# Kernel tuning notes

Measured on AMD Instinct MI355X. Metric: run time of the kernel, lower is better.

## Reference

```python
import jax, jax.numpy as jnp
import numpy as np

MIN_PS = 4
MAX_PS = 16


def _enforce(mb):
    # mb: (L,) bool candidate boundaries (merge_signal < 0.7-quantile)
    # Faithful re-implementation of _enforce_patch_size_constraints:
    # walk boundaries left->right, skip segments < MIN_PS (start not advanced),
    # accept otherwise, and insert ceil(ps/MAX_PS)-1 evenly spaced splits for
    # oversized segments. seq_len-1 is always appended as a candidate.
    L = mb.shape[0]
    pos = jnp.arange(L, dtype=jnp.int32)
    cand = mb | (pos == L - 1)

    def fwd_step(start, inp):
        p, is_c = inp
        ps = p - start
        acc = is_c & (ps >= MIN_PS)
        k = jnp.where(acc, (ps + MAX_PS - 1) // MAX_PS, jnp.int32(1))
        sz = jnp.maximum(jnp.where(acc, ps // k, jnp.int32(1)), 1)
        new_start = jnp.where(acc, p, start)
        return new_start, (acc, start, sz, k)

    _, (acc, seg_start, sz, k) = jax.lax.scan(fwd_step, jnp.int32(0), (pos, cand))

    # Reverse scan: propagate each accepted boundary's (start, split_size, num_splits)
    # back to the interior positions of its segment so splits can be placed in parallel.
    def rev_step(carry, inp):
        a, s, z, kk = inp
        cs, cz, ck, cv = carry
        out = (cs, cz, ck, cv)
        ncarry = (jnp.where(a, s, cs), jnp.where(a, z, cz), jnp.where(a, kk, ck), cv | a)
        return ncarry, out

    init = (jnp.int32(0), jnp.int32(1), jnp.int32(1), jnp.bool_(False))
    _, (fs, fz, fk, fv) = jax.lax.scan(rev_step, init, (acc, seg_start, sz, k), reverse=True)
    r = pos - fs
    j = r // fz
    split = fv & (r > 0) & (r % fz == 0) & (j >= 1) & (j <= fk - 1)
    return acc | split


def reference(x, attention_mask, W1, b1, W2, b2, Wc, bc, Wb1, bb1, Wb2, bb2):
    B, L, D = x.shape
    # content scorer: Linear -> ReLU -> Linear -> Sigmoid
    content = jax.nn.sigmoid(jax.nn.relu(x @ W1 + b1) @ W2 + b2)[..., 0]  # (B, L)
    # grouped Conv1d(d, d//2, k=3, pad=1, groups=d//4)
    xc = jnp.transpose(x, (0, 2, 1))  # (B, D, L)
    pf = jax.lax.conv_general_dilated(xc, Wc, (1,), ((1, 1),),
                                      feature_group_count=D // 4,
                                      dimension_numbers=('NCH', 'OIH', 'NCH'))
    pf = jnp.transpose(pf + bc[None, :, None], (0, 2, 1))  # (B, L, D//2)
    comb = jnp.concatenate([x, pf], axis=-1)
    bscore = jax.nn.sigmoid(jax.nn.relu(comb @ Wb1 + bb1) @ Wb2 + bb2)[..., 0]  # (B, L)
    signal = content * (1.0 - bscore) * attention_mask
    thr = jnp.quantile(signal, 0.7, axis=1, keepdims=True)
    mb = signal < thr
    new_b = jax.vmap(_enforce)(mb)  # (B, L) bool, new_b[:,0] is always False

    # segment id per token = inclusive cumsum of boundaries
    seg = jnp.cumsum(new_b.astype(jnp.int32), axis=1)
    seg_flat = (seg + jnp.arange(B, dtype=jnp.int32)[:, None] * L).reshape(-1)
    NS = B * L
    xm = x * attention_mask[..., None]
    e = jnp.sum(xm * xm, axis=-1).reshape(-1)  # softmax logits = ||token||^2
    m = jax.ops.segment_max(e, seg_flat, num_segments=NS)
    w = jnp.exp(e - m[seg_flat])
    denom = jax.ops.segment_sum(w, seg_flat, num_segments=NS)
    wn = w / denom[seg_flat]
    merged = jax.ops.segment_sum(xm.reshape(-1, D) * wn[:, None], seg_flat,
                                 num_segments=NS).reshape(B, L, D)
    # segment_boundaries: 1 for every segment except the first, zero padding
    n_last = seg[:, -1]
    p = jnp.arange(L)
    seg_bounds = ((p[None, :] >= 1) & (p[None, :] <= n_last[:, None])).astype(jnp.float32)
    return merged, seg_bounds


def setup_inputs() -> dict:
    key = jax.random.key(0)
    B, L, D = 4, 8192, 512
    ks = jax.random.split(key, 8)
    s = 0.02
    return {
        'x': jax.random.normal(ks[0], (B, L, D), jnp.float32),
        'attention_mask': jnp.ones((B, L), jnp.float32),
        'W1': jax.random.normal(ks[1], (D, D // 4), jnp.float32) * s,
        'b1': jnp.zeros((D // 4,), jnp.float32),
        'W2': jax.random.normal(ks[2], (D // 4, 1), jnp.float32) * s,
        'b2': jnp.zeros((1,), jnp.float32),
        'Wc': jax.random.normal(ks[3], (D // 2, 4, 3), jnp.float32) * s,
        'bc': jnp.zeros((D // 2,), jnp.float32),
        'Wb1': jax.random.normal(ks[4], (D + D // 2, D // 4), jnp.float32) * s,
        'bb1': jnp.zeros((D // 4,), jnp.float32),
        'Wb2': jax.random.normal(ks[5], (D // 4, 1), jnp.float32) * s,
        'bb2': jnp.zeros((1,), jnp.float32),
    }
```

## Files before the change

### kernel.cpp

```cpp
#include <hip/hip_runtime.h>
#include <math.h>

#define B_  4
#define L_  8192
#define D_  512
#define BL_ (B_*L_)
#define TOK 32
#define XS  36
#define KC  16
#define NCH (D_/KC)

__global__ __launch_bounds__(256, 4) void k_signal(
    const float* __restrict__ x, const float* __restrict__ mask,
    const float* __restrict__ W1, const float* __restrict__ b1,
    const float* __restrict__ W2, const float* __restrict__ b2,
    const float* __restrict__ Wc, const float* __restrict__ bc,
    const float* __restrict__ Wb1, const float* __restrict__ bb1,
    const float* __restrict__ Wb2, const float* __restrict__ bb2,
    float* __restrict__ signal, float* __restrict__ e)
{
  __shared__ float ws1[KC][128];
  __shared__ float wsb[KC][128];
  __shared__ float wsp[8][128];
  __shared__ float xt[KC][XS];
  __shared__ float pf[8][XS];

  const int t   = threadIdx.x;
  const int blk = blockIdx.x;
  const int b   = blk >> 8;
  const int l0  = (blk & 255) * TOK;
  const float* xb = x + (size_t)b * L_ * D_;

  const int jq = t & 31, tw = t >> 5;
  const int j0 = jq << 2, tok0 = tw << 2;

  const int stok = t >> 2, skk = t & 3;
  const int oo_c  = t >> 5;
  const int tokc  = t & 31;
  const int cb_c  = (oo_c >> 1) << 2;

  const int row = t >> 5, c4 = (t & 31) << 2;

  float a1[4][4], a2[4][4];
#pragma unroll
  for (int i = 0; i < 4; ++i)
#pragma unroll
    for (int j = 0; j < 4; ++j) { a1[i][j] = 0.f; a2[i][j] = 0.f; }
  float esacc = 0.f;

  float4 r_w1a, r_w1b, r_wba, r_wbb, r_wp, r_x;
  float4 r_wc0, r_wc1, r_wc2;
  float  r_bc;

#define ISSUE_LOADS(cc) do {                                                    \
    const int kc_ = (cc) << 4;                                                  \
    r_w1a = *reinterpret_cast<const float4*>(W1 + (size_t)(kc_ + row) * 128 + c4);       \
    r_w1b = *reinterpret_cast<const float4*>(W1 + (size_t)(kc_ + 8 + row) * 128 + c4);   \
    r_wba = *reinterpret_cast<const float4*>(Wb1 + (size_t)(kc_ + row) * 128 + c4);      \
    r_wbb = *reinterpret_cast<const float4*>(Wb1 + (size_t)(kc_ + 8 + row) * 128 + c4);  \
    r_wp  = *reinterpret_cast<const float4*>(Wb1 + (size_t)(512 + ((cc) << 3) + row) * 128 + c4); \
    {                                                                           \
      const int o_ = ((cc) << 3) + oo_c;                                        \
      const float* wcp_ = Wc + o_ * 12;                                         \
      r_wc0 = *reinterpret_cast<const float4*>(wcp_);                           \
      r_wc1 = *reinterpret_cast<const float4*>(wcp_ + 4);                       \
      r_wc2 = *reinterpret_cast<const float4*>(wcp_ + 8);                       \
      r_bc  = bc[o_];                                                           \
    }                                                                           \
    if (t < 128) {                                                              \
      r_x = *reinterpret_cast<const float4*>(xb + (size_t)(l0 + stok) * D_ + kc_ + (skk << 2)); \
    } else if (t < 136) {                                                       \
      const int q_ = t - 128;                                                   \
      const int l_ = (q_ >> 2) ? (l0 + TOK) : (l0 - 1);                         \
      r_x = make_float4(0.f, 0.f, 0.f, 0.f);                                    \
      if (l_ >= 0 && l_ < L_)                                                   \
        r_x = *reinterpret_cast<const float4*>(xb + (size_t)l_ * D_ + kc_ + ((q_ & 3) << 2)); \
    }                                                                           \
  } while (0)

#define WRITE_LDS() do {                                                        \
    *reinterpret_cast<float4*>(&ws1[row][c4]) = r_w1a;                          \
    *reinterpret_cast<float4*>(&ws1[8 + row][c4]) = r_w1b;                      \
    *reinterpret_cast<float4*>(&wsb[row][c4]) = r_wba;                          \
    *reinterpret_cast<float4*>(&wsb[8 + row][c4]) = r_wbb;                      \
    *reinterpret_cast<float4*>(&wsp[row][c4]) = r_wp;                           \
    if (t < 128) {                                                              \
      esacc = fmaf(r_x.x, r_x.x, esacc); esacc = fmaf(r_x.y, r_x.y, esacc);     \
      esacc = fmaf(r_x.z, r_x.z, esacc); esacc = fmaf(r_x.w, r_x.w, esacc);     \
      const int r_ = skk << 2;                                                  \
      xt[r_ + 0][stok] = r_x.x; xt[r_ + 1][stok] = r_x.y;                       \
      xt[r_ + 2][stok] = r_x.z; xt[r_ + 3][stok] = r_x.w;                       \
    } else if (t < 136) {                                                       \
      const int q_ = t - 128; const int kk_ = q_ & 3;                           \
      const int col_ = TOK + (q_ >> 2); const int r_ = kk_ << 2;                \
      xt[r_ + 0][col_] = r_x.x; xt[r_ + 1][col_] = r_x.y;                       \
      xt[r_ + 2][col_] = r_x.z; xt[r_ + 3][col_] = r_x.w;                       \
    }                                                                           \
  } while (0)

  ISSUE_LOADS(0);
  WRITE_LDS();

  for (int c = 0; c < NCH; ++c) {
    __syncthreads();

    {
      const float wc12[12] = {r_wc0.x, r_wc0.y, r_wc0.z, r_wc0.w,
                              r_wc1.x, r_wc1.y, r_wc1.z, r_wc1.w,
                              r_wc2.x, r_wc2.y, r_wc2.z, r_wc2.w};
      float acc = r_bc;
      const int tm1 = (tokc == 0) ? TOK : tokc - 1;
      const int tp1 = (tokc == TOK - 1) ? TOK + 1 : tokc + 1;
#pragma unroll
      for (int i = 0; i < 4; ++i) {
        const float* rowp = &xt[cb_c + i][0];
        acc = fmaf(rowp[tm1],  wc12[i * 3 + 0], acc);
        acc = fmaf(rowp[tokc], wc12[i * 3 + 1], acc);
        acc = fmaf(rowp[tp1],  wc12[i * 3 + 2], acc);
      }
      pf[oo_c][tokc] = acc;
    }

    if (c + 1 < NCH) ISSUE_LOADS(c + 1);

#pragma unroll 4
    for (int k = 0; k < KC; ++k) {
      const float4 w1 = *reinterpret_cast<const float4*>(&ws1[k][j0]);
      const float4 wb = *reinterpret_cast<const float4*>(&wsb[k][j0]);
      const float4 xv = *reinterpret_cast<const float4*>(&xt[k][tok0]);
      const float xs4[4] = {xv.x, xv.y, xv.z, xv.w};
#pragma unroll
      for (int i = 0; i < 4; ++i) {
        a1[i][0] = fmaf(xs4[i], w1.x, a1[i][0]);
        a1[i][1] = fmaf(xs4[i], w1.y, a1[i][1]);
        a1[i][2] = fmaf(xs4[i], w1.z, a1[i][2]);
        a1[i][3] = fmaf(xs4[i], w1.w, a1[i][3]);
        a2[i][0] = fmaf(xs4[i], wb.x, a2[i][0]);
        a2[i][1] = fmaf(xs4[i], wb.y, a2[i][1]);
        a2[i][2] = fmaf(xs4[i], wb.z, a2[i][2]);
        a2[i][3] = fmaf(xs4[i], wb.w, a2[i][3]);
      }
    }
    __syncthreads();

#pragma unroll 4
    for (int oo = 0; oo < 8; ++oo) {
      const float4 wp = *reinterpret_cast<const float4*>(&wsp[oo][j0]);
      const float4 pv = *reinterpret_cast<const float4*>(&pf[oo][tok0]);
      const float ps4[4] = {pv.x, pv.y, pv.z, pv.w};
#pragma unroll
      for (int i = 0; i < 4; ++i) {
        a2[i][0] = fmaf(ps4[i], wp.x, a2[i][0]);
        a2[i][1] = fmaf(ps4[i], wp.y, a2[i][1]);
        a2[i][2] = fmaf(ps4[i], wp.z, a2[i][2]);
        a2[i][3] = fmaf(ps4[i], wp.w, a2[i][3]);
      }
    }

    if (c + 1 < NCH) {
      __syncthreads();
      WRITE_LDS();
    }
  }

  {
    float b1v[4], w2v[4], bbv[4], wv2[4];
#pragma unroll
    for (int jj = 0; jj < 4; ++jj) {
      b1v[jj] = b1[j0 + jj];  w2v[jj] = W2[j0 + jj];
      bbv[jj] = bb1[j0 + jj]; wv2[jj] = Wb2[j0 + jj];
    }
    const float bias2 = b2[0], biasb2 = bb2[0];
#pragma unroll
    for (int i = 0; i < 4; ++i) {
      float p1 = 0.f, p2 = 0.f;
#pragma unroll
      for (int jj = 0; jj < 4; ++jj) {
        const float h1 = a1[i][jj] + b1v[jj];
        if (h1 > 0.f) p1 = fmaf(h1, w2v[jj], p1);
        const float h2 = a2[i][jj] + bbv[jj];
        if (h2 > 0.f) p2 = fmaf(h2, wv2[jj], p2);
      }
#pragma unroll
      for (int off = 1; off < 32; off <<= 1) {
        p1 += __shfl_xor(p1, off, 64);
        p2 += __shfl_xor(p2, off, 64);
      }
      if (jq == 0) {
        const int gi = b * L_ + l0 + tok0 + i;
        const float content = 1.f / (1.f + expf(-(p1 + bias2)));
        const float bscore  = 1.f / (1.f + expf(-(p2 + biasb2)));
        signal[gi] = content * (1.f - bscore) * mask[gi];
      }
    }
  }

  if (t < 128) {
    float es = esacc;
    es += __shfl_xor(es, 1, 64);
    es += __shfl_xor(es, 2, 64);
    if (skk == 0) {
      const int gi = b * L_ + l0 + stok;
      const float m = mask[gi];
      e[gi] = m * m * es;
    }
  }
#undef ISSUE_LOADS
#undef WRITE_LDS
}

__device__ __forceinline__ int chain_sim(unsigned long long w, int from) {
  int last = -1;
  while (from < 64) {
    const unsigned long long m = w & (~0ull << from);
    if (m == 0ull) break;
    const int p = __ffsll(m) - 1;
    last = p;
    from = p + 4;
  }
  return last;
}

__global__ __launch_bounds__(1024) void k_select(
    const float* __restrict__ signal,
    int* __restrict__ starts, int* __restrict__ nlast, float* __restrict__ bounds)
{
  __shared__ unsigned int bins[4][256];
  __shared__ unsigned int sel_prefix;
  __shared__ int sel_rank;
  __shared__ float sh_thr;
  __shared__ unsigned int wmin[16];
  __shared__ int wcnt[16];
  __shared__ unsigned long long cw[128];
  __shared__ unsigned char nb[L_];
  __shared__ signed char tbl[128][4];
  __shared__ int st_in[128];
  __shared__ int tsum[256];
  __shared__ int offs[257];

  const int b = blockIdx.x, t = threadIdx.x;
  const int wv = t >> 6, lane = t & 63;
  const float* s = signal + b * L_;

  float val[8];
  unsigned int key[8];
#pragma unroll
  for (int i = 0; i < 8; ++i) {
    val[i] = s[(i << 10) + t];
    const unsigned int u = __float_as_uint(val[i]);
    key[i] = (u & 0x80000000u) ? ~u : (u | 0x80000000u);
  }

  if (t == 0) { sel_prefix = 0u; sel_rank = 5733; }
  __syncthreads();
  for (int round = 0; round < 4; ++round) {
    reinterpret_cast<unsigned int*>(bins)[t] = 0u;
    __syncthreads();
    const unsigned int pre = sel_prefix;
    const int shift = 24 - 8 * round;
    if (round < 2) {
#pragma unroll
      for (int i = 0; i < 8; ++i) {
        const bool act = (round == 0) || ((key[i] >> (shift + 8)) == pre);
        const unsigned int bin = (key[i] >> shift) & 255u;
        unsigned long long peers = __ballot(act);
#pragma unroll
        for (int bit = 0; bit < 8; ++bit) {
          const bool myb = (bin >> bit) & 1;
          const unsigned long long bb = __ballot(act && myb);
          peers &= myb ? bb : ~bb;
        }
        if (act) {
          const int leader = __ffsll(peers) - 1;
          if (lane == leader)
            atomicAdd(&bins[wv >> 2][bin], (unsigned int)__popcll(peers));
        }
      }
    } else {
#pragma unroll
      for (int i = 0; i < 8; ++i) {
        if ((key[i] >> (shift + 8)) == pre)
          atomicAdd(&bins[wv >> 2][(key[i] >> shift) & 255u], 1u);
      }
    }
    __syncthreads();
    if (t < 256)
      bins[0][t] = bins[0][t] + bins[1][t] + bins[2][t] + bins[3][t];
    __syncthreads();
    if (t < 64) {
      const unsigned int c0 = bins[0][(t << 2) + 0], c1 = bins[0][(t << 2) + 1];
      const unsigned int c2 = bins[0][(t << 2) + 2], c3 = bins[0][(t << 2) + 3];
      const unsigned int lsum = c0 + c1 + c2 + c3;
      unsigned int run = lsum;
#pragma unroll
      for (int off = 1; off < 64; off <<= 1) {
        const unsigned int v = __shfl_up(run, off, 64);
        if (t >= off) run += v;
      }
      const int r = sel_rank;
      if (r >= (int)(run - lsum) && r < (int)run) {
        int rr = r - (int)(run - lsum);
        unsigned int cbin;
        if (rr < (int)c0) { cbin = 0; }
        else if (rr < (int)(c0 + c1)) { cbin = 1; rr -= (int)c0; }
        else if (rr < (int)(c0 + c1 + c2)) { cbin = 2; rr -= (int)(c0 + c1); }
        else { cbin = 3; rr -= (int)(c0 + c1 + c2); }
        sel_rank = rr;
        sel_prefix = (pre << 8) | ((unsigned int)(t << 2) | cbin);
      }
    }
    __syncthreads();
  }
  const unsigned int k0 = sel_prefix;

  {
    int cle = 0;
    unsigned int mgt = 0xFFFFFFFFu;
#pragma unroll
    for (int i = 0; i < 8; ++i) {
      if (key[i] <= k0) ++cle;
      else mgt = min(mgt, key[i]);
    }
#pragma unroll
    for (int off = 1; off < 64; off <<= 1) {
      cle += __shfl_xor(cle, off, 64);
      mgt = min(mgt, (unsigned int)__shfl_xor((int)mgt, off, 64));
    }
    if (lane == 0) { wcnt[wv] = cle; wmin[wv] = mgt; }
    __syncthreads();
    if (t == 0) {
      int C = 0; unsigned int M = 0xFFFFFFFFu;
      for (int g = 0; g < 16; ++g) { C += wcnt[g]; M = min(M, wmin[g]); }
      const unsigned int k1 = (C >= 5735) ? k0 : M;
      const unsigned int u0 = (k0 & 0x80000000u) ? (k0 & 0x7fffffffu) : ~k0;
      const unsigned int u1 = (k1 & 0x80000000u) ? (k1 & 0x7fffffffu) : ~k1;
      const float v0 = __uint_as_float(u0);
      const float v1 = __uint_as_float(u1);
      const float g = 0.7f * 8191.0f - 5733.0f;
      sh_thr = v0 + g * (v1 - v0);
    }
    __syncthreads();
  }
  const float thr = sh_thr;

#pragma unroll
  for (int i = 0; i < 8; ++i) {
    const unsigned long long m = __ballot(val[i] < thr);
    if (lane == 0) cw[(i << 4) + wv] = m;
  }
  {
    const int base = t << 3;
#pragma unroll
    for (int i = 0; i < 8; ++i) nb[base + i] = 0;
  }
  __syncthreads();
  if (t == 0) cw[127] |= (1ull << 63);
  __syncthreads();

  if (t < 512) {
    const int blk = t >> 2, cls = t & 3;
    tbl[blk][cls] = (signed char)chain_sim(cw[blk], cls);
  }
  __syncthreads();

  if (t == 0) {
    int st = 0;
    for (int blk = 0; blk < 128; ++blk) {
      const int bs = blk << 6;
      st_in[blk] = st;
      int pl;
      if (blk == 0) {
        pl = chain_sim(cw[0], 4);
      } else {
        int off = st + 4 - bs;
        if (off < 0) off = 0;
        pl = tbl[blk][off];
      }
      if (pl >= 0) st = bs + pl;
    }
  }
  __syncthreads();

  if (t < 128) {
    const int bs = t << 6;
    const unsigned long long w = cw[t];
    int st = st_in[t];
    int from = st + 4 - bs;
    if (from < 0) from = 0;
    while (from < 64) {
      const unsigned long long m = w & (~0ull << from);
      if (m == 0ull) break;
      const int p_rel = __ffsll(m) - 1;
      const int p = bs + p_rel;
      nb[p] = 1;
      const int ps = p - st;
      const int k = (ps + 15) >> 4;
      if (k > 1) {
        int sz = ps / k; if (sz < 1) sz = 1;
        for (int j = 1; j < k; ++j) nb[st + j * sz] = 1;
      }
      st = p;
      from = p_rel + 4;
    }
  }
  __syncthreads();

  if (t < 256) {
    const int base = t << 5;
    int ls = 0;
    for (int i = 0; i < 32; ++i) ls += nb[base + i];
    tsum[t] = ls;
  }
  __syncthreads();
  if (t == 0) {
    int r = 0;
    for (int i = 0; i < 256; ++i) { offs[i] = r; r += tsum[i]; }
    offs[256] = r;
  }
  __syncthreads();
  if (t < 256) {
    const int base = t << 5;
    int run = offs[t];
    for (int i = 0; i < 32; ++i) {
      run += nb[base + i];
      if (nb[base + i]) starts[b * L_ + run] = base + i;
    }
  }
  if (t == 0) { starts[b * L_ + 0] = 0; nlast[b] = offs[256]; }
  __syncthreads();
  const int total = offs[256];
  for (int i = t; i < L_; i += 1024)
    bounds[b * L_ + i] = (i >= 1 && i <= total) ? 1.0f : 0.0f;
}

__global__ __launch_bounds__(64) void k_merge(const float* __restrict__ x,
    const float* __restrict__ mask, const float* __restrict__ e,
    const int* __restrict__ starts, const int* __restrict__ nlast,
    float* __restrict__ merged)
{
  const int idx = blockIdx.x;
  const int b   = idx >> 13;
  const int sid = idx & (L_ - 1);
  const int n = nlast[b];
  const int lane = threadIdx.x;
  const int c0 = lane << 3;
  float* o = merged + (size_t)(b * L_ + sid) * D_ + c0;
  if (sid > n) {
    const float4 z = make_float4(0.f, 0.f, 0.f, 0.f);
    reinterpret_cast<float4*>(o)[0] = z;
    reinterpret_cast<float4*>(o)[1] = z;
    return;
  }
  const int t0 = starts[b * L_ + sid];
  const int t1 = (sid < n) ? starts[b * L_ + sid + 1] : L_;
  const float* eb = e + b * L_;

  float mx = -INFINITY;
  for (int p = t0; p < t1; ++p) mx = fmaxf(mx, eb[p]);
  float den = 0.f;
  for (int p = t0; p < t1; ++p) den += expf(eb[p] - mx);

  float acc[8] = {0,0,0,0,0,0,0,0};
  for (int p = t0; p < t1; ++p) {
    const float wn = expf(eb[p] - mx) / den;
    const float sc = wn * mask[b * L_ + p];
    const float* xr = x + ((size_t)(b * L_ + p)) * D_ + c0;
    const float4 u0 = reinterpret_cast<const float4*>(xr)[0];
    const float4 u1 = reinterpret_cast<const float4*>(xr)[1];
    acc[0] = fmaf(sc, u0.x, acc[0]); acc[1] = fmaf(sc, u0.y, acc[1]);
    acc[2] = fmaf(sc, u0.z, acc[2]); acc[3] = fmaf(sc, u0.w, acc[3]);
    acc[4] = fmaf(sc, u1.x, acc[4]); acc[5] = fmaf(sc, u1.y, acc[5]);
    acc[6] = fmaf(sc, u1.z, acc[6]); acc[7] = fmaf(sc, u1.w, acc[7]);
  }
  reinterpret_cast<float4*>(o)[0] = make_float4(acc[0], acc[1], acc[2], acc[3]);
  reinterpret_cast<float4*>(o)[1] = make_float4(acc[4], acc[5], acc[6], acc[7]);
}

extern "C" void kernel_launch(void* const* d_in, const int* in_sizes, int n_in,
                              void* d_out, int out_size, void* d_ws, size_t ws_size,
                              hipStream_t stream) {
  (void)in_sizes; (void)n_in; (void)out_size; (void)ws_size;
  const float* x    = (const float*)d_in[0];
  const float* mask = (const float*)d_in[1];
  const float* W1   = (const float*)d_in[2];
  const float* b1   = (const float*)d_in[3];
  const float* W2   = (const float*)d_in[4];
  const float* b2   = (const float*)d_in[5];
  const float* Wc   = (const float*)d_in[6];
  const float* bc   = (const float*)d_in[7];
  const float* Wb1  = (const float*)d_in[8];
  const float* bb1  = (const float*)d_in[9];
  const float* Wb2  = (const float*)d_in[10];
  const float* bb2  = (const float*)d_in[11];

  float* merged = (float*)d_out;
  float* bounds = (float*)d_out + (size_t)BL_ * D_;

  char* ws = (char*)d_ws;
  float* signal = (float*)(ws);
  float* e      = (float*)(ws + (size_t)BL_ * 4);
  int*   starts = (int*)  (ws + (size_t)BL_ * 8);
  int*   nlast  = (int*)  (ws + (size_t)BL_ * 12);

  k_signal<<<BL_ / TOK, 256, 0, stream>>>(x, mask, W1, b1, W2, b2, Wc, bc,
                                          Wb1, bb1, Wb2, bb2, signal, e);
  k_select<<<B_, 1024, 0, stream>>>(signal, starts, nlast, bounds);
  k_merge<<<BL_, 64, 0, stream>>>(x, mask, e, starts, nlast, merged);
}
```

Baseline: 318.1 us.

## Use async global-to-LDS weight loads, double-buffer wsp, and parallelize merge softmax

In k_signal, the W1/Wb1 chunks now go straight from global memory into LDS through global_load_lds. This removes the register staging and one barrier per chunk, and wsp is double-buffered so the next chunk's projection weights can load while the current one is used. Launch bounds are raised to 5 blocks per CU. k_merge now packs 4 wavefronts per block, computes the segment max and sum with wave reductions instead of serial loops, and prefetches the next x row. The risks are async-load ordering hazards (the loads are not explicitly waited on before the barrier), extra register pressure, and load imbalance across segments of varying length.

```diff
diff --git a/kernel.cpp b/kernel.cpp
--- a/kernel.cpp
+++ b/kernel.cpp
@@ -10,7 +10,12 @@
 #define KC  16
 #define NCH (D_/KC)
 
-__global__ __launch_bounds__(256, 4) void k_signal(
+#define ASYNC16(gp, lp)                                                   \
+  __builtin_amdgcn_global_load_lds(                                       \
+      (const __attribute__((address_space(1))) void*)(gp),                \
+      (__attribute__((address_space(3))) void*)(lp), 16, 0, 0)
+
+__global__ __launch_bounds__(256, 5) void k_signal(
     const float* __restrict__ x, const float* __restrict__ mask,
     const float* __restrict__ W1, const float* __restrict__ b1,
     const float* __restrict__ W2, const float* __restrict__ b2,
@@ -21,7 +26,7 @@
 {
   __shared__ float ws1[KC][128];
   __shared__ float wsb[KC][128];
-  __shared__ float wsp[8][128];
+  __shared__ float wsp[2][8][128];
   __shared__ float xt[KC][XS];
   __shared__ float pf[8][XS];
 
@@ -39,8 +44,6 @@
   const int tokc  = t & 31;
   const int cb_c  = (oo_c >> 1) << 2;
 
-  const int row = t >> 5, c4 = (t & 31) << 2;
-
   float a1[4][4], a2[4][4];
 #pragma unroll
   for (int i = 0; i < 4; ++i)
@@ -48,42 +51,44 @@
     for (int j = 0; j < 4; ++j) { a1[i][j] = 0.f; a2[i][j] = 0.f; }
   float esacc = 0.f;
 
-  float4 r_w1a, r_w1b, r_wba, r_wbb, r_wp, r_x;
-  float4 r_wc0, r_wc1, r_wc2;
+  float4 r_x, r_wc0, r_wc1, r_wc2;
   float  r_bc;
 
-#define ISSUE_LOADS(cc) do {                                                    \
+#define ISSUE_WEIGHTS(cc) do {                                                  \
     const int kc_ = (cc) << 4;                                                  \
-    r_w1a = *reinterpret_cast<const float4*>(W1 + (size_t)(kc_ + row) * 128 + c4);       \
-    r_w1b = *reinterpret_cast<const float4*>(W1 + (size_t)(kc_ + 8 + row) * 128 + c4);   \
-    r_wba = *reinterpret_cast<const float4*>(Wb1 + (size_t)(kc_ + row) * 128 + c4);      \
-    r_wbb = *reinterpret_cast<const float4*>(Wb1 + (size_t)(kc_ + 8 + row) * 128 + c4);  \
-    r_wp  = *reinterpret_cast<const float4*>(Wb1 + (size_t)(512 + ((cc) << 3) + row) * 128 + c4); \
-    {                                                                           \
-      const int o_ = ((cc) << 3) + oo_c;                                        \
-      const float* wcp_ = Wc + o_ * 12;                                         \
-      r_wc0 = *reinterpret_cast<const float4*>(wcp_);                           \
-      r_wc1 = *reinterpret_cast<const float4*>(wcp_ + 4);                       \
-      r_wc2 = *reinterpret_cast<const float4*>(wcp_ + 8);                       \
-      r_bc  = bc[o_];                                                           \
-    }                                                                           \
+    const float* g1 = W1  + (size_t)kc_ * 128 + (t << 2);                       \
+    const float* gb = Wb1 + (size_t)kc_ * 128 + (t << 2);                       \
+    const float* gp = Wb1 + (size_t)(512 + ((cc) << 3)) * 128 + (t << 2);       \
+    float* l1 = &ws1[0][0] + ((t >> 6) << 8);                                   \
+    float* lb = &wsb[0][0] + ((t >> 6) << 8);                                   \
+    float* lp = &wsp[(cc) & 1][0][0] + ((t >> 6) << 8);                         \
+    ASYNC16(g1, l1);  ASYNC16(g1 + 1024, l1 + 1024);                            \
+    ASYNC16(gb, lb);  ASYNC16(gb + 1024, lb + 1024);                            \
+    ASYNC16(gp, lp);                                                            \
+  } while (0)
+
+#define LOAD_REGS(cc) do {                                                      \
+    const int kc_ = (cc) << 4;                                                  \
+    const int o_ = ((cc) << 3) + oo_c;                                          \
+    const float* wcp_ = Wc + o_ * 12;                                           \
+    r_wc0 = *reinterpret_cast<const float4*>(wcp_);                             \
+    r_wc1 = *reinterpret_cast<const float4*>(wcp_ + 4);                         \
+    r_wc2 = *reinterpret_cast<const float4*>(wcp_ + 8);                         \
+    r_bc  = bc[o_];                                                             \
     if (t < 128) {                                                              \
-      r_x = *reinterpret_cast<const float4*>(xb + (size_t)(l0 + stok) * D_ + kc_ + (skk << 2)); \
+      r_x = *reinterpret_cast<const float4*>(                                   \
+          xb + (size_t)(l0 + stok) * D_ + kc_ + (skk << 2));                    \
     } else if (t < 136) {                                                       \
       const int q_ = t - 128;                                                   \
       const int l_ = (q_ >> 2) ? (l0 + TOK) : (l0 - 1);                         \
       r_x = make_float4(0.f, 0.f, 0.f, 0.f);                                    \
       if (l_ >= 0 && l_ < L_)                                                   \
-        r_x = *reinterpret_cast<const float4*>(xb + (size_t)l_ * D_ + kc_ + ((q_ & 3) << 2)); \
+        r_x = *reinterpret_cast<const float4*>(                                 \
+            xb + (size_t)l_ * D_ + kc_ + ((q_ & 3) << 2));                      \
     }                                                                           \
   } while (0)
 
-#define WRITE_LDS() do {                                                        \
-    *reinterpret_cast<float4*>(&ws1[row][c4]) = r_w1a;                          \
-    *reinterpret_cast<float4*>(&ws1[8 + row][c4]) = r_w1b;                      \
-    *reinterpret_cast<float4*>(&wsb[row][c4]) = r_wba;                          \
-    *reinterpret_cast<float4*>(&wsb[8 + row][c4]) = r_wbb;                      \
-    *reinterpret_cast<float4*>(&wsp[row][c4]) = r_wp;                           \
+#define WRITE_XT() do {                                                         \
     if (t < 128) {                                                              \
       esacc = fmaf(r_x.x, r_x.x, esacc); esacc = fmaf(r_x.y, r_x.y, esacc);     \
       esacc = fmaf(r_x.z, r_x.z, esacc); esacc = fmaf(r_x.w, r_x.w, esacc);     \
@@ -98,8 +103,9 @@
     }                                                                           \
   } while (0)
 
-  ISSUE_LOADS(0);
-  WRITE_LDS();
+  ISSUE_WEIGHTS(0);
+  LOAD_REGS(0);
+  WRITE_XT();
 
   for (int c = 0; c < NCH; ++c) {
     __syncthreads();
@@ -120,8 +126,6 @@
       }
       pf[oo_c][tokc] = acc;
     }
-
-    if (c + 1 < NCH) ISSUE_LOADS(c + 1);
 
 #pragma unroll 4
     for (int k = 0; k < KC; ++k) {
@@ -143,24 +147,29 @@
     }
     __syncthreads();
 
+    if (c + 1 < NCH) {
+      ISSUE_WEIGHTS(c + 1);
+      LOAD_REGS(c + 1);
+    }
+
+    {
+      const float (*wspc)[128] = wsp[c & 1];
 #pragma unroll 4
-    for (int oo = 0; oo < 8; ++oo) {
-      const float4 wp = *reinterpret_cast<const float4*>(&wsp[oo][j0]);
-      const float4 pv = *reinterpret_cast<const float4*>(&pf[oo][tok0]);
-      const float ps4[4] = {pv.x, pv.y, pv.z, pv.w};
-#pragma unroll
-      for (int i = 0; i < 4; ++i) {
-        a2[i][0] = fmaf(ps4[i], wp.x, a2[i][0]);
-        a2[i][1] = fmaf(ps4[i], wp.y, a2[i][1]);
-        a2[i][2] = fmaf(ps4[i], wp.z, a2[i][2]);
-        a2[i][3] = fmaf(ps4[i], wp.w, a2[i][3]);
-      }
-    }
-
-    if (c + 1 < NCH) {
-      __syncthreads();
-      WRITE_LDS();
-    }
+      for (int oo = 0; oo < 8; ++oo) {
+        const float4 wp = *reinterpret_cast<const float4*>(&wspc[oo][j0]);
+        const float4 pv = *reinterpret_cast<const float4*>(&pf[oo][tok0]);
+        const float ps4[4] = {pv.x, pv.y, pv.z, pv.w};
+#pragma unroll
+        for (int i = 0; i < 4; ++i) {
+          a2[i][0] = fmaf(ps4[i], wp.x, a2[i][0]);
+          a2[i][1] = fmaf(ps4[i], wp.y, a2[i][1]);
+          a2[i][2] = fmaf(ps4[i], wp.z, a2[i][2]);
+          a2[i][3] = fmaf(ps4[i], wp.w, a2[i][3]);
+        }
+      }
+    }
+
+    if (c + 1 < NCH) WRITE_XT();
   }
 
   {
@@ -205,8 +214,9 @@
       e[gi] = m * m * es;
     }
   }
-#undef ISSUE_LOADS
-#undef WRITE_LDS
+#undef ISSUE_WEIGHTS
+#undef LOAD_REGS
+#undef WRITE_XT
 }
 
 __device__ __forceinline__ int chain_sim(unsigned long long w, int from) {
@@ -433,16 +443,16 @@
     bounds[b * L_ + i] = (i >= 1 && i <= total) ? 1.0f : 0.0f;
 }
 
-__global__ __launch_bounds__(64) void k_merge(const float* __restrict__ x,
+__global__ __launch_bounds__(256) void k_merge(const float* __restrict__ x,
     const float* __restrict__ mask, const float* __restrict__ e,
     const int* __restrict__ starts, const int* __restrict__ nlast,
     float* __restrict__ merged)
 {
-  const int idx = blockIdx.x;
+  const int wv = threadIdx.x >> 6, lane = threadIdx.x & 63;
+  const int idx = (blockIdx.x << 2) + wv;
   const int b   = idx >> 13;
   const int sid = idx & (L_ - 1);
   const int n = nlast[b];
-  const int lane = threadIdx.x;
   const int c0 = lane << 3;
   float* o = merged + (size_t)(b * L_ + sid) * D_ + c0;
   if (sid > n) {
@@ -453,24 +463,53 @@
   }
   const int t0 = starts[b * L_ + sid];
   const int t1 = (sid < n) ? starts[b * L_ + sid + 1] : L_;
+  const int len = t1 - t0;
   const float* eb = e + b * L_;
+  const float* mk = mask + b * L_;
 
   float mx = -INFINITY;
-  for (int p = t0; p < t1; ++p) mx = fmaxf(mx, eb[p]);
-  float den = 0.f;
-  for (int p = t0; p < t1; ++p) den += expf(eb[p] - mx);
-
+  for (int base = 0; base < len; base += 64) {
+    const int p = base + lane;
+    float m = (p < len) ? eb[t0 + p] : -INFINITY;
+#pragma unroll
+    for (int off = 32; off > 0; off >>= 1)
+      m = fmaxf(m, __shfl_xor(m, off, 64));
+    mx = fmaxf(mx, m);
+  }
+  float den = 0.f, w0 = 0.f;
+  for (int base = 0; base < len; base += 64) {
+    const int p = base + lane;
+    float w = (p < len) ? expf(eb[t0 + p] - mx) : 0.f;
+    if (base == 0) w0 = w;
+    float sthis = w;
+#pragma unroll
+    for (int off = 32; off > 0; off >>= 1)
+      sthis += __shfl_xor(sthis, off, 64);
+    den += sthis;
+  }
   float acc[8] = {0,0,0,0,0,0,0,0};
-  for (int p = t0; p < t1; ++p) {
-    const float wn = expf(eb[p] - mx) / den;
-    const float sc = wn * mask[b * L_ + p];
-    const float* xr = x + ((size_t)(b * L_ + p)) * D_ + c0;
-    const float4 u0 = reinterpret_cast<const float4*>(xr)[0];
-    const float4 u1 = reinterpret_cast<const float4*>(xr)[1];
-    acc[0] = fmaf(sc, u0.x, acc[0]); acc[1] = fmaf(sc, u0.y, acc[1]);
-    acc[2] = fmaf(sc, u0.z, acc[2]); acc[3] = fmaf(sc, u0.w, acc[3]);
-    acc[4] = fmaf(sc, u1.x, acc[4]); acc[5] = fmaf(sc, u1.y, acc[5]);
-    acc[6] = fmaf(sc, u1.z, acc[6]); acc[7] = fmaf(sc, u1.w, acc[7]);
+  for (int base = 0; base < len; base += 64) {
+    const int p = base + lane;
+    const float w = (base == 0) ? w0 : ((p < len) ? expf(eb[t0 + p] - mx) : 0.f);
+    const float scl = (p < len) ? (w / den) * mk[t0 + p] : 0.f;
+    const int cnt = (len - base < 64) ? (len - base) : 64;
+    const float* xr0 = x + (size_t)(b * L_ + t0 + base) * D_ + c0;
+    float4 u0 = reinterpret_cast<const float4*>(xr0)[0];
+    float4 u1 = reinterpret_cast<const float4*>(xr0)[1];
+    for (int q = 0; q < cnt; ++q) {
+      float4 v0, v1;
+      if (q + 1 < cnt) {
+        const float* xr = xr0 + (size_t)(q + 1) * D_;
+        v0 = reinterpret_cast<const float4*>(xr)[0];
+        v1 = reinterpret_cast<const float4*>(xr)[1];
+      }
+      const float sc = __shfl(scl, q, 64);
+      acc[0] = fmaf(sc, u0.x, acc[0]); acc[1] = fmaf(sc, u0.y, acc[1]);
+      acc[2] = fmaf(sc, u0.z, acc[2]); acc[3] = fmaf(sc, u0.w, acc[3]);
+      acc[4] = fmaf(sc, u1.x, acc[4]); acc[5] = fmaf(sc, u1.y, acc[5]);
+      acc[6] = fmaf(sc, u1.z, acc[6]); acc[7] = fmaf(sc, u1.w, acc[7]);
+      u0 = v0; u1 = v1;
+    }
   }
   reinterpret_cast<float4*>(o)[0] = make_float4(acc[0], acc[1], acc[2], acc[3]);
   reinterpret_cast<float4*>(o)[1] = make_float4(acc[4], acc[5], acc[6], acc[7]);
@@ -505,5 +544,5 @@
   k_signal<<<BL_ / TOK, 256, 0, stream>>>(x, mask, W1, b1, W2, b2, Wc, bc,
                                           Wb1, bb1, Wb2, bb2, signal, e);
   k_select<<<B_, 1024, 0, stream>>>(signal, starts, nlast, bounds);
-  k_merge<<<BL_, 64, 0, stream>>>(x, mask, e, starts, nlast, merged);
+  k_merge<<<BL_ / 4, 256, 0, stream>>>(x, mask, e, starts, nlast, merged);
 }
```

After: 316.5 us. About the same (-0.5%).
